# Optimization experiments

Hardware: AMD Instinct MI355X
Metric: run time of the kernel (lower is better)

Reference implementation:

```python
import jax, jax.numpy as jnp
import numpy as np

SEQ, B, I, H, L = 2048, 32, 1024, 1024, 2


def setup_inputs() -> dict:
    key = jax.random.key(0)
    ks = jax.random.split(key, 6)
    k = 1.0 / np.sqrt(H)
    x = jax.random.normal(ks[0], (SEQ, B, I), dtype=jnp.float32)
    h0 = jnp.zeros((L, B, H), dtype=jnp.float32)
    # layer 0 W_ih is [H, I]; with I == H all layers stack to [L, H, H]
    W_ih = jax.random.uniform(ks[1], (L, H, H), minval=-k, maxval=k, dtype=jnp.float32)
    W_hh = jax.random.uniform(ks[2], (L, H, H), minval=-k, maxval=k, dtype=jnp.float32)
    b_ih = jax.random.uniform(ks[3], (L, H), minval=-k, maxval=k, dtype=jnp.float32)
    b_hh = jax.random.uniform(ks[4], (L, H), minval=-k, maxval=k, dtype=jnp.float32)
    return {"x": x, "h0": h0, "W_ih": W_ih, "W_hh": W_hh, "b_ih": b_ih, "b_hh": b_hh}


def reference(x, h0, W_ih, W_hh, b_ih, b_hh):
    """Stacked tanh RNN, seq-first input [T, B, I]. Returns (h_history [T,B,H], h_T [L,B,H])."""
    num_layers = W_ih.shape[0]

    def step(h_prev, x_t):
        inp = x_t
        hs = []
        for l in range(num_layers):  # small fixed layer count
            a = (jnp.einsum('bd,cd->bc', inp, W_ih[l])
                 + jnp.einsum('bd,cd->bc', h_prev[l], W_hh[l])
                 + b_ih[l] + b_hh[l])
            hl = jnp.tanh(a)
            hs.append(hl)
            inp = hl
        h_new = jnp.stack(hs)  # [L, B, H]
        return h_new, h_new[-1]

    h_T, h_history = jax.lax.scan(step, h0, x)
    return h_history, h_T
```

## Files before the change

### kernel.cpp

```cpp
#include <hip/hip_runtime.h>
#include <stdint.h>

#define T_SEQ 2048
#define NB 32
#define NH 1024
#define HH (NH*NH)
#define HIST_ELEMS ((size_t)T_SEQ*NB*NH)
#define TEAM 32

typedef __attribute__((ext_vector_type(8))) short bf16x8;
typedef __attribute__((ext_vector_type(4))) float f32x4;
typedef __attribute__((ext_vector_type(4))) int   i32x4;
typedef __attribute__((ext_vector_type(2))) int   i32x2;
typedef __attribute__((ext_vector_type(4))) short s16x4;

__device__ __forceinline__ unsigned short bf16rne(float f){
  union { float f; unsigned u; } v; v.f = f;
  unsigned u = v.u;
  return (unsigned short)((u + 0x7FFFu + ((u >> 16) & 1u)) >> 16);
}
__device__ __forceinline__ float bf16tof(unsigned short s){
  union { unsigned u; float f; } v; v.u = ((unsigned)s) << 16; return v.f;
}
__device__ __forceinline__ float fast_tanh(float x){
  float ax = fabsf(x);
  float e  = __expf(-2.0f*ax);
  float t  = (1.0f - e) / (1.0f + e);
  return copysignf(t, x);
}

__device__ __forceinline__ i32x4 ld128_c(const void* p){
  i32x4 d;
  asm volatile("global_load_dwordx4 %0, %1, off sc0 sc1" : "=v"(d) : "v"(p) : "memory");
  return d;
}
__device__ __forceinline__ void st64_c(void* p, i32x2 v){
  asm volatile("global_store_dwordx2 %0, %1, off sc0 sc1" :: "v"(p), "v"(v) : "memory");
}
__device__ __forceinline__ unsigned ld32_c(const void* p){
  unsigned d;
  asm volatile("global_load_dword %0, %1, off sc0 sc1\n\ts_waitcnt vmcnt(0)"
               : "=v"(d) : "v"(p) : "memory");
  __builtin_amdgcn_sched_barrier(0);
  return d;
}
__device__ __forceinline__ void vmem_drain(){
  asm volatile("s_waitcnt vmcnt(0)" ::: "memory");
  __builtin_amdgcn_sched_barrier(0);
}

__global__ __launch_bounds__(256)
void pre_gemm(const float* __restrict__ x,
              const float* __restrict__ Wih,
              const float* __restrict__ bih,
              const float* __restrict__ bhh,
              _Float16* __restrict__ pre0)
{
  __shared__ float As[128][36];
  const int tid  = threadIdx.x;
  const int lane = tid & 63;
  const int wave = tid >> 6;
  const int l15  = lane & 15;
  const int l4   = lane >> 4;
  const int n0   = blockIdx.x * 128;
  const int m0   = blockIdx.y * 128;
  const int qm   = wave >> 1;
  const int qn   = wave & 1;

  f32x4 acc[4][4];
  #pragma unroll
  for (int i = 0; i < 4; ++i)
    #pragma unroll
    for (int j = 0; j < 4; ++j) acc[i][j] = (f32x4){0.f,0.f,0.f,0.f};

  const int sr = tid >> 1;
  const int sh = tid & 1;
  const float* xrow = x + (size_t)(m0 + sr)*NH + sh*16;

  for (int kb = 0; kb < 32; ++kb){
    __syncthreads();
    {
      const float* src = xrow + kb*32;
      f32x4 v0 = *(const f32x4*)(src + 0);
      f32x4 v1 = *(const f32x4*)(src + 4);
      f32x4 v2 = *(const f32x4*)(src + 8);
      f32x4 v3 = *(const f32x4*)(src + 12);
      float* dst = &As[sr][sh*16];
      *(f32x4*)(dst + 0)  = v0;
      *(f32x4*)(dst + 4)  = v1;
      *(f32x4*)(dst + 8)  = v2;
      *(f32x4*)(dst + 12) = v3;
    }
    __syncthreads();

    bf16x8 ahi[4], alo[4];
    #pragma unroll
    for (int mt = 0; mt < 4; ++mt){
      const float* ap = &As[64*qm + 16*mt + l15][l4*8];
      #pragma unroll
      for (int j = 0; j < 8; ++j){
        float a = ap[j];
        unsigned short hb = bf16rne(a);
        ahi[mt][j] = (short)hb;
        alo[mt][j] = (short)bf16rne(a - bf16tof(hb));
      }
    }
    #pragma unroll
    for (int nf = 0; nf < 4; ++nf){
      const int c = n0 + 64*qn + 16*nf + l15;
      const float* wp = Wih + (size_t)c*NH + kb*32 + l4*8;
      bf16x8 bf;
      #pragma unroll
      for (int j = 0; j < 8; ++j) bf[j] = (short)bf16rne(wp[j]);
      #pragma unroll
      for (int mt = 0; mt < 4; ++mt){
        acc[mt][nf] = __builtin_amdgcn_mfma_f32_16x16x32_bf16(ahi[mt], bf, acc[mt][nf], 0,0,0);
        acc[mt][nf] = __builtin_amdgcn_mfma_f32_16x16x32_bf16(alo[mt], bf, acc[mt][nf], 0,0,0);
      }
    }
  }

  #pragma unroll
  for (int nf = 0; nf < 4; ++nf){
    const int c = n0 + 64*qn + 16*nf + l15;
    const float bv = bih[c] + bhh[c];
    #pragma unroll
    for (int mt = 0; mt < 4; ++mt){
      const int mb = m0 + 64*qm + 16*mt + l4*4;
      #pragma unroll
      for (int j = 0; j < 4; ++j)
        pre0[(size_t)(mb + j)*NH + c] = (_Float16)(acc[mt][nf][j] + bv);
    }
  }
}

__global__ __launch_bounds__(256, 1)
void rnn_seq(const float* __restrict__ h0in,
             const float* __restrict__ Wih,
             const float* __restrict__ Whh,
             const float* __restrict__ bih,
             const float* __restrict__ bhh,
             const _Float16* __restrict__ pre0,
             float* __restrict__ dout,
             char* __restrict__ ws)
{
  const int tid  = threadIdx.x;
  const int lane = tid & 63;
  const int wave = tid >> 6;
  const int l15  = lane & 15;
  const int l4   = lane >> 4;
  const int rank = blockIdx.x;
  const int c0   = rank * 32;

  unsigned* flags = (unsigned*)ws;
  char* H0 = ws + 8192;
  char* H1 = ws + 8192 + 131072;

  bf16x8 wA[3][2][8];
  #pragma unroll
  for (int cf = 0; cf < 2; ++cf){
    const size_t row = (size_t)(c0 + cf*16 + l15) * NH;
    const float* s0 = Whh + row;
    const float* s1 = Wih + HH + row;
    const float* s2 = Whh + HH + row;
    #pragma unroll
    for (int s = 0; s < 8; ++s){
      const int k = wave*256 + s*32 + l4*8;
      #pragma unroll
      for (int j = 0; j < 8; ++j){
        wA[0][cf][s][j] = (short)bf16rne(s0[k+j]);
        wA[1][cf][s][j] = (short)bf16rne(s1[k+j]);
        wA[2][cf][s][j] = (short)bf16rne(s2[k+j]);
      }
    }
  }

  const int eb   = tid >> 3;
  const int ecb  = tid & 7;
  const int ecol = c0 + ecb*4;

  f32x4 bias1;
  #pragma unroll
  for (int j = 0; j < 4; ++j)
    bias1[j] = bih[NH + ecol + j] + bhh[NH + ecol + j];

  {
    const float* hs0 = h0in + (size_t)eb*NH + ecol;
    const float* hs1 = h0in + (size_t)NB*NH + (size_t)eb*NH + ecol;
    i32x2 p0, p1;
    p0[0] = (int)bf16rne(hs0[0]) | ((int)bf16rne(hs0[1]) << 16);
    p0[1] = (int)bf16rne(hs0[2]) | ((int)bf16rne(hs0[3]) << 16);
    p1[0] = (int)bf16rne(hs1[0]) | ((int)bf16rne(hs1[1]) << 16);
    p1[1] = (int)bf16rne(hs1[2]) | ((int)bf16rne(hs1[3]) << 16);
    st64_c(H0 + 65536 + eb*2048 + ecol*2, p0);
    st64_c(H1 + 65536 + eb*2048 + ecol*2, p1);
  }
  vmem_drain();
  if (lane == 0) atomicAdd(&flags[rank*32], 1u);

  __shared__ float scr[4][8][16][20];
  long spins = 0;

  for (int p = 0; p <= T_SEQ; ++p){
    const bool doL0 = (p < T_SEQ);
    const bool doL1 = (p >= 1);

    s16x4 praw = {0,0,0,0};
    if (doL0)
      praw = *(const s16x4*)(pre0 + (size_t)p*(NB*NH) + (size_t)eb*NH + ecol);

    {
      const unsigned target = 4u * (unsigned)(p + 1);
      const unsigned* fp = flags + (lane & 31)*32;
      for (;;){
        unsigned f = ld32_c(fp);
        int ok = (lane >= 32) || (f >= target);
        if (__all(ok)) break;
        if (++spins > (1L << 21)) break;
        if (spins > 4096) __builtin_amdgcn_s_sleep(1);
      }
    }

    const char* h0rd = H0 + ((p-1)&1)*65536;
    const char* h1rd = H1 + ((p-2)&1)*65536;
    i32x4 g0[2][8], g1[2][8];
    #pragma unroll
    for (int bt = 0; bt < 2; ++bt){
      const int b = bt*16 + l15;
      #pragma unroll
      for (int s = 0; s < 8; ++s){
        const int d = wave*256 + s*32 + l4*8;
        g0[bt][s] = ld128_c(h0rd + b*2048 + d*2);
      }
    }
    if (doL1){
      #pragma unroll
      for (int bt = 0; bt < 2; ++bt){
        const int b = bt*16 + l15;
        #pragma unroll
        for (int s = 0; s < 8; ++s){
          const int d = wave*256 + s*32 + l4*8;
          g1[bt][s] = ld128_c(h1rd + b*2048 + d*2);
        }
      }
    }
    vmem_drain();

    f32x4 acc0[2][2] = {{{0,0,0,0},{0,0,0,0}},{{0,0,0,0},{0,0,0,0}}};
    f32x4 acc1[2][2] = {{{0,0,0,0},{0,0,0,0}},{{0,0,0,0},{0,0,0,0}}};
    #pragma unroll
    for (int cf = 0; cf < 2; ++cf){
      #pragma unroll
      for (int bt = 0; bt < 2; ++bt){
        #pragma unroll
        for (int s = 0; s < 8; ++s){
          bf16x8 b0 = __builtin_bit_cast(bf16x8, g0[bt][s]);
          if (doL0)
            acc0[cf][bt] = __builtin_amdgcn_mfma_f32_16x16x32_bf16(wA[0][cf][s], b0, acc0[cf][bt], 0,0,0);
          if (doL1){
            acc1[cf][bt] = __builtin_amdgcn_mfma_f32_16x16x32_bf16(wA[1][cf][s], b0, acc1[cf][bt], 0,0,0);
            bf16x8 b1 = __builtin_bit_cast(bf16x8, g1[bt][s]);
            acc1[cf][bt] = __builtin_amdgcn_mfma_f32_16x16x32_bf16(wA[2][cf][s], b1, acc1[cf][bt], 0,0,0);
          }
        }
      }
    }

    #pragma unroll
    for (int cf = 0; cf < 2; ++cf){
      #pragma unroll
      for (int bt = 0; bt < 2; ++bt){
        *(f32x4*)&scr[wave][(cf<<1)|bt][l15][l4*4]   = acc0[cf][bt];
        *(f32x4*)&scr[wave][4|(cf<<1)|bt][l15][l4*4] = acc1[cf][bt];
      }
    }
    __syncthreads();

    const int fL0 = ((ecb >> 2) << 1) | (eb >> 4);
    f32x4 s0v = {0,0,0,0}, s1v = {0,0,0,0};
    #pragma unroll
    for (int w = 0; w < 4; ++w){
      s0v += *(const f32x4*)&scr[w][fL0][eb & 15][(ecb & 3)*4];
      s1v += *(const f32x4*)&scr[w][4|fL0][eb & 15][(ecb & 3)*4];
    }

    float hv0[4], hv1[4];
    if (doL0){
      union { s16x4 v; _Float16 h[4]; } pu; pu.v = praw;
      #pragma unroll
      for (int j = 0; j < 4; ++j)
        hv0[j] = fast_tanh(s0v[j] + (float)pu.h[j]);
      i32x2 pk;
      pk[0] = (int)bf16rne(hv0[0]) | ((int)bf16rne(hv0[1]) << 16);
      pk[1] = (int)bf16rne(hv0[2]) | ((int)bf16rne(hv0[3]) << 16);
      st64_c(H0 + (p&1)*65536 + eb*2048 + ecol*2, pk);
    }
    if (doL1){
      #pragma unroll
      for (int j = 0; j < 4; ++j)
        hv1[j] = fast_tanh(s1v[j] + bias1[j]);
      i32x2 pk;
      pk[0] = (int)bf16rne(hv1[0]) | ((int)bf16rne(hv1[1]) << 16);
      pk[1] = (int)bf16rne(hv1[2]) | ((int)bf16rne(hv1[3]) << 16);
      st64_c(H1 + ((p-1)&1)*65536 + eb*2048 + ecol*2, pk);
    }

    vmem_drain();
    if (lane == 0) atomicAdd(&flags[rank*32], 1u);

    if (doL1){
      f32x4 o = {hv1[0], hv1[1], hv1[2], hv1[3]};
      *(f32x4*)(dout + (size_t)(p-1)*(NB*NH) + (size_t)eb*NH + ecol) = o;
      if (p == T_SEQ)
        *(f32x4*)(dout + HIST_ELEMS + (size_t)NB*NH + (size_t)eb*NH + ecol) = o;
    }
    if (doL0 && p == T_SEQ-1){
      f32x4 o = {hv0[0], hv0[1], hv0[2], hv0[3]};
      *(f32x4*)(dout + HIST_ELEMS + (size_t)eb*NH + ecol) = o;
    }
  }
}

extern "C" void kernel_launch(void* const* d_in, const int* in_sizes, int n_in,
                              void* d_out, int out_size, void* d_ws, size_t ws_size,
                              hipStream_t stream)
{
  (void)in_sizes; (void)n_in; (void)out_size;
  const float* x   = (const float*)d_in[0];
  const float* h0  = (const float*)d_in[1];
  const float* Wih = (const float*)d_in[2];
  const float* Whh = (const float*)d_in[3];
  const float* bih = (const float*)d_in[4];
  const float* bhh = (const float*)d_in[5];
  float* out = (float*)d_out;
  char*  ws  = (char*)d_ws;

  const size_t PRE0_OFF = (size_t)1 << 20;
  const size_t NEED = PRE0_OFF + (size_t)T_SEQ*NB*NH*sizeof(_Float16);
  if (ws_size < NEED) return;

  _Float16* pre0 = (_Float16*)(ws + PRE0_OFF);

  hipMemsetAsync(ws, 0, 4096, stream);
  pre_gemm<<<dim3(8, 512), 256, 0, stream>>>(x, Wih, bih, bhh, pre0);
  rnn_seq<<<dim3(TEAM), 256, 0, stream>>>(h0, Wih, Whh, bih, bhh, pre0, out, ws);
}
```

Before: 15.75 ms.

## Replace flag-counter barrier with per-element tagged hidden-state exchange

Removes the global atomic flag counters and the drain-then-signal handshake between the 32 persistent blocks. Each bf16 hidden value is now stored in a 32-bit word together with a 16-bit step tag, and consumers spin on the tags, validating every gathered word before use. Layer 1 can now start on its recurrent term as soon as its own data is ready instead of waiting for all producers. The cost is double the exchange traffic, extra unpack and validation ALU work, and a larger workspace memset.

```diff
diff --git a/kernel.cpp b/kernel.cpp
--- a/kernel.cpp
+++ b/kernel.cpp
@@ -7,11 +7,11 @@
 #define HH (NH*NH)
 #define HIST_ELEMS ((size_t)T_SEQ*NB*NH)
 #define TEAM 32
+#define SLOTB (NB*NH*4)
 
 typedef __attribute__((ext_vector_type(8))) short bf16x8;
 typedef __attribute__((ext_vector_type(4))) float f32x4;
 typedef __attribute__((ext_vector_type(4))) int   i32x4;
-typedef __attribute__((ext_vector_type(2))) int   i32x2;
 typedef __attribute__((ext_vector_type(4))) short s16x4;
 
 __device__ __forceinline__ unsigned short bf16rne(float f){
@@ -29,25 +29,86 @@
   return copysignf(t, x);
 }
 
-__device__ __forceinline__ i32x4 ld128_c(const void* p){
-  i32x4 d;
-  asm volatile("global_load_dwordx4 %0, %1, off sc0 sc1" : "=v"(d) : "v"(p) : "memory");
-  return d;
-}
-__device__ __forceinline__ void st64_c(void* p, i32x2 v){
-  asm volatile("global_store_dwordx2 %0, %1, off sc0 sc1" :: "v"(p), "v"(v) : "memory");
-}
-__device__ __forceinline__ unsigned ld32_c(const void* p){
+__device__ __forceinline__ void st128_c(void* p, i32x4 v){
+  asm volatile("global_store_dwordx4 %0, %1, off sc0 sc1" :: "v"(p), "v"(v) : "memory");
+}
+
+__device__ __forceinline__ unsigned probe32(const void* p){
   unsigned d;
   asm volatile("global_load_dword %0, %1, off sc0 sc1\n\ts_waitcnt vmcnt(0)"
-               : "=v"(d) : "v"(p) : "memory");
+               : "=&v"(d) : "v"(p) : "memory");
   __builtin_amdgcn_sched_barrier(0);
   return d;
 }
-__device__ __forceinline__ void vmem_drain(){
-  asm volatile("s_waitcnt vmcnt(0)" ::: "memory");
-  __builtin_amdgcn_sched_barrier(0);
-}
+
+__device__ __forceinline__ i32x4 pack_frag(const i32x4 a, const i32x4 b,
+                                           unsigned rep, unsigned &bad){
+  unsigned a0=(unsigned)a[0], a1=(unsigned)a[1], a2=(unsigned)a[2], a3=(unsigned)a[3];
+  unsigned b0=(unsigned)b[0], b1=(unsigned)b[1], b2=(unsigned)b[2], b3=(unsigned)b[3];
+  i32x4 f;
+  f[0] = (int)((a0 >> 16) | (a1 & 0xFFFF0000u));
+  f[1] = (int)((a2 >> 16) | (a3 & 0xFFFF0000u));
+  f[2] = (int)((b0 >> 16) | (b1 & 0xFFFF0000u));
+  f[3] = (int)((b2 >> 16) | (b3 & 0xFFFF0000u));
+  bad |= ((a0 & 0xFFFFu) | (a1 << 16)) ^ rep;
+  bad |= ((a2 & 0xFFFFu) | (a3 << 16)) ^ rep;
+  bad |= ((b0 & 0xFFFFu) | (b1 << 16)) ^ rep;
+  bad |= ((b2 & 0xFFFFu) | (b3 << 16)) ^ rep;
+  return f;
+}
+
+#define GATHER16(RB, FARR, REP, BAD)                                         \
+  {                                                                          \
+    i32x4 r0,r1,r2,r3,r4,r5,r6,r7,r8,r9,r10,r11,r12,r13,r14,r15;             \
+    asm volatile(                                                            \
+      "global_load_dwordx4 %0, %16, off sc0 sc1\n\t"                         \
+      "global_load_dwordx4 %1, %16, off offset:16 sc0 sc1\n\t"               \
+      "global_load_dwordx4 %2, %16, off offset:128 sc0 sc1\n\t"              \
+      "global_load_dwordx4 %3, %16, off offset:144 sc0 sc1\n\t"              \
+      "global_load_dwordx4 %4, %16, off offset:256 sc0 sc1\n\t"              \
+      "global_load_dwordx4 %5, %16, off offset:272 sc0 sc1\n\t"              \
+      "global_load_dwordx4 %6, %16, off offset:384 sc0 sc1\n\t"              \
+      "global_load_dwordx4 %7, %16, off offset:400 sc0 sc1\n\t"              \
+      "global_load_dwordx4 %8, %16, off offset:512 sc0 sc1\n\t"              \
+      "global_load_dwordx4 %9, %16, off offset:528 sc0 sc1\n\t"              \
+      "global_load_dwordx4 %10, %16, off offset:640 sc0 sc1\n\t"             \
+      "global_load_dwordx4 %11, %16, off offset:656 sc0 sc1\n\t"             \
+      "global_load_dwordx4 %12, %16, off offset:768 sc0 sc1\n\t"             \
+      "global_load_dwordx4 %13, %16, off offset:784 sc0 sc1\n\t"             \
+      "global_load_dwordx4 %14, %16, off offset:896 sc0 sc1\n\t"             \
+      "global_load_dwordx4 %15, %16, off offset:912 sc0 sc1\n\t"             \
+      "s_waitcnt vmcnt(0)"                                                   \
+      : "=&v"(r0),"=&v"(r1),"=&v"(r2),"=&v"(r3),                             \
+        "=&v"(r4),"=&v"(r5),"=&v"(r6),"=&v"(r7),                             \
+        "=&v"(r8),"=&v"(r9),"=&v"(r10),"=&v"(r11),                           \
+        "=&v"(r12),"=&v"(r13),"=&v"(r14),"=&v"(r15)                          \
+      : "v"(RB) : "memory");                                                 \
+    __builtin_amdgcn_sched_barrier(0);                                       \
+    FARR[0] = pack_frag(r0,r1,REP,BAD);   FARR[1] = pack_frag(r2,r3,REP,BAD);   \
+    FARR[2] = pack_frag(r4,r5,REP,BAD);   FARR[3] = pack_frag(r6,r7,REP,BAD);   \
+    FARR[4] = pack_frag(r8,r9,REP,BAD);   FARR[5] = pack_frag(r10,r11,REP,BAD); \
+    FARR[6] = pack_frag(r12,r13,REP,BAD); FARR[7] = pack_frag(r14,r15,REP,BAD); \
+  }
+
+#define WAIT_GATHER(BASE, FARR, REP, TAG)                                    \
+  {                                                                          \
+    int pw = 0;                                                              \
+    for (;;){                                                                \
+      unsigned pr = probe32(BASE);                                           \
+      if (__all((int)((pr & 0xFFFFu) == (TAG)))) break;                      \
+      if (++pw > 8192) break;                                                \
+      if (pw > 8) __builtin_amdgcn_s_sleep(1);                               \
+    }                                                                        \
+    int gt = 0;                                                              \
+    for (;;){                                                                \
+      unsigned bad = 0;                                                      \
+      GATHER16(BASE,         FARR[0], REP, bad);                             \
+      GATHER16(BASE + 65536, FARR[1], REP, bad);                             \
+      if (__all((int)(bad == 0))) break;                                     \
+      if (++gt > 1024) break;                                                \
+      if (gt > 4) __builtin_amdgcn_s_sleep(1);                               \
+    }                                                                        \
+  }
 
 __global__ __launch_bounds__(256)
 void pre_gemm(const float* __restrict__ x,
@@ -152,9 +213,8 @@
   const int rank = blockIdx.x;
   const int c0   = rank * 32;
 
-  unsigned* flags = (unsigned*)ws;
-  char* H0 = ws + 8192;
-  char* H1 = ws + 8192 + 131072;
+  char* H0 = ws + 4096;
+  char* H1 = ws + 4096 + 2*SLOTB;
 
   bf16x8 wA[3][2][8];
   #pragma unroll
@@ -187,19 +247,19 @@
   {
     const float* hs0 = h0in + (size_t)eb*NH + ecol;
     const float* hs1 = h0in + (size_t)NB*NH + (size_t)eb*NH + ecol;
-    i32x2 p0, p1;
-    p0[0] = (int)bf16rne(hs0[0]) | ((int)bf16rne(hs0[1]) << 16);
-    p0[1] = (int)bf16rne(hs0[2]) | ((int)bf16rne(hs0[3]) << 16);
-    p1[0] = (int)bf16rne(hs1[0]) | ((int)bf16rne(hs1[1]) << 16);
-    p1[1] = (int)bf16rne(hs1[2]) | ((int)bf16rne(hs1[3]) << 16);
-    st64_c(H0 + 65536 + eb*2048 + ecol*2, p0);
-    st64_c(H1 + 65536 + eb*2048 + ecol*2, p1);
-  }
-  vmem_drain();
-  if (lane == 0) atomicAdd(&flags[rank*32], 1u);
+    i32x4 p0, p1;
+    #pragma unroll
+    for (int j = 0; j < 4; ++j){
+      p0[j] = (int)((((unsigned)bf16rne(hs0[j])) << 16) | 1u);
+      p1[j] = (int)((((unsigned)bf16rne(hs1[j])) << 16) | 1u);
+    }
+    st128_c(H0 + SLOTB + (size_t)(eb*NH + ecol)*4, p0);
+    st128_c(H1 + SLOTB + (size_t)(eb*NH + ecol)*4, p1);
+  }
 
   __shared__ float scr[4][8][16][20];
-  long spins = 0;
+
+  const size_t gofs = (size_t)l15*4096 + (size_t)wave*1024 + (size_t)l4*32;
 
   for (int p = 0; p <= T_SEQ; ++p){
     const bool doL0 = (p < T_SEQ);
@@ -209,63 +269,48 @@
     if (doL0)
       praw = *(const s16x4*)(pre0 + (size_t)p*(NB*NH) + (size_t)eb*NH + ecol);
 
-    {
-      const unsigned target = 4u * (unsigned)(p + 1);
-      const unsigned* fp = flags + (lane & 31)*32;
-      for (;;){
-        unsigned f = ld32_c(fp);
-        int ok = (lane >= 32) || (f >= target);
-        if (__all(ok)) break;
-        if (++spins > (1L << 21)) break;
-        if (spins > 4096) __builtin_amdgcn_s_sleep(1);
-      }
-    }
-
-    const char* h0rd = H0 + ((p-1)&1)*65536;
-    const char* h1rd = H1 + ((p-2)&1)*65536;
-    i32x4 g0[2][8], g1[2][8];
-    #pragma unroll
-    for (int bt = 0; bt < 2; ++bt){
-      const int b = bt*16 + l15;
-      #pragma unroll
-      for (int s = 0; s < 8; ++s){
-        const int d = wave*256 + s*32 + l4*8;
-        g0[bt][s] = ld128_c(h0rd + b*2048 + d*2);
-      }
-    }
-    if (doL1){
-      #pragma unroll
-      for (int bt = 0; bt < 2; ++bt){
-        const int b = bt*16 + l15;
-        #pragma unroll
-        for (int s = 0; s < 8; ++s){
-          const int d = wave*256 + s*32 + l4*8;
-          g1[bt][s] = ld128_c(h1rd + b*2048 + d*2);
-        }
-      }
-    }
-    vmem_drain();
-
     f32x4 acc0[2][2] = {{{0,0,0,0},{0,0,0,0}},{{0,0,0,0},{0,0,0,0}}};
     f32x4 acc1[2][2] = {{{0,0,0,0},{0,0,0,0}},{{0,0,0,0},{0,0,0,0}}};
-    #pragma unroll
-    for (int cf = 0; cf < 2; ++cf){
-      #pragma unroll
-      for (int bt = 0; bt < 2; ++bt){
+
+    if (doL1){
+      const char* base = H1 + (size_t)((p-2)&1)*SLOTB + gofs;
+      const unsigned tag = (unsigned)p;
+      const unsigned rep = tag * 0x10001u;
+      i32x4 f1[2][8];
+      WAIT_GATHER(base, f1, rep, tag);
+      #pragma unroll
+      for (int cf = 0; cf < 2; ++cf)
         #pragma unroll
-        for (int s = 0; s < 8; ++s){
-          bf16x8 b0 = __builtin_bit_cast(bf16x8, g0[bt][s]);
-          if (doL0)
-            acc0[cf][bt] = __builtin_amdgcn_mfma_f32_16x16x32_bf16(wA[0][cf][s], b0, acc0[cf][bt], 0,0,0);
-          if (doL1){
-            acc1[cf][bt] = __builtin_amdgcn_mfma_f32_16x16x32_bf16(wA[1][cf][s], b0, acc1[cf][bt], 0,0,0);
-            bf16x8 b1 = __builtin_bit_cast(bf16x8, g1[bt][s]);
-            acc1[cf][bt] = __builtin_amdgcn_mfma_f32_16x16x32_bf16(wA[2][cf][s], b1, acc1[cf][bt], 0,0,0);
+        for (int bt = 0; bt < 2; ++bt)
+          #pragma unroll
+          for (int s = 0; s < 8; ++s)
+            acc1[cf][bt] = __builtin_amdgcn_mfma_f32_16x16x32_bf16(
+                wA[2][cf][s], __builtin_bit_cast(bf16x8, f1[bt][s]), acc1[cf][bt], 0,0,0);
+    }
+
+    {
+      const char* base = H0 + (size_t)((p-1)&1)*SLOTB + gofs;
+      const unsigned tag = (unsigned)(p + 1);
+      const unsigned rep = tag * 0x10001u;
+      i32x4 f0[2][8];
+      WAIT_GATHER(base, f0, rep, tag);
+      #pragma unroll
+      for (int cf = 0; cf < 2; ++cf){
+        #pragma unroll
+        for (int bt = 0; bt < 2; ++bt){
+          #pragma unroll
+          for (int s = 0; s < 8; ++s){
+            bf16x8 b0 = __builtin_bit_cast(bf16x8, f0[bt][s]);
+            if (doL0)
+              acc0[cf][bt] = __builtin_amdgcn_mfma_f32_16x16x32_bf16(wA[0][cf][s], b0, acc0[cf][bt], 0,0,0);
+            if (doL1)
+              acc1[cf][bt] = __builtin_amdgcn_mfma_f32_16x16x32_bf16(wA[1][cf][s], b0, acc1[cf][bt], 0,0,0);
           }
         }
       }
     }
 
+    __syncthreads();
     #pragma unroll
     for (int cf = 0; cf < 2; ++cf){
       #pragma unroll
@@ -284,29 +329,28 @@
       s1v += *(const f32x4*)&scr[w][4|fL0][eb & 15][(ecb & 3)*4];
     }
 
+    const unsigned wtag0 = (unsigned)(p + 2);
+    const unsigned wtag1 = (unsigned)(p + 1);
     float hv0[4], hv1[4];
     if (doL0){
       union { s16x4 v; _Float16 h[4]; } pu; pu.v = praw;
-      #pragma unroll
-      for (int j = 0; j < 4; ++j)
+      i32x4 pk;
+      #pragma unroll
+      for (int j = 0; j < 4; ++j){
         hv0[j] = fast_tanh(s0v[j] + (float)pu.h[j]);
-      i32x2 pk;
-      pk[0] = (int)bf16rne(hv0[0]) | ((int)bf16rne(hv0[1]) << 16);
-      pk[1] = (int)bf16rne(hv0[2]) | ((int)bf16rne(hv0[3]) << 16);
-      st64_c(H0 + (p&1)*65536 + eb*2048 + ecol*2, pk);
+        pk[j] = (int)((((unsigned)bf16rne(hv0[j])) << 16) | wtag0);
+      }
+      st128_c(H0 + (size_t)(p&1)*SLOTB + (size_t)(eb*NH + ecol)*4, pk);
     }
     if (doL1){
-      #pragma unroll
-      for (int j = 0; j < 4; ++j)
+      i32x4 pk;
+      #pragma unroll
+      for (int j = 0; j < 4; ++j){
         hv1[j] = fast_tanh(s1v[j] + bias1[j]);
-      i32x2 pk;
-      pk[0] = (int)bf16rne(hv1[0]) | ((int)bf16rne(hv1[1]) << 16);
-      pk[1] = (int)bf16rne(hv1[2]) | ((int)bf16rne(hv1[3]) << 16);
-      st64_c(H1 + ((p-1)&1)*65536 + eb*2048 + ecol*2, pk);
-    }
-
-    vmem_drain();
-    if (lane == 0) atomicAdd(&flags[rank*32], 1u);
+        pk[j] = (int)((((unsigned)bf16rne(hv1[j])) << 16) | wtag1);
+      }
+      st128_c(H1 + (size_t)((p-1)&1)*SLOTB + (size_t)(eb*NH + ecol)*4, pk);
+    }
 
     if (doL1){
       f32x4 o = {hv1[0], hv1[1], hv1[2], hv1[3]};
@@ -341,7 +385,7 @@
 
   _Float16* pre0 = (_Float16*)(ws + PRE0_OFF);
 
-  hipMemsetAsync(ws, 0, 4096, stream);
+  hipMemsetAsync(ws, 0, 4096 + 4*(size_t)SLOTB, stream);
   pre_gemm<<<dim3(8, 512), 256, 0, stream>>>(x, Wih, bih, bhh, pre0);
   rnn_seq<<<dim3(TEAM), 256, 0, stream>>>(h0, Wih, Whh, bih, bhh, pre0, out, ws);
 }
```

New measurement: 30.48 ms. 1.94x slower.
